# Optimization experiments

Hardware: AMD Instinct MI355X
Metric: run time of the kernel (lower is better)

## Reference

```python
import jax, jax.numpy as jnp
import numpy as np

N, E_EDGES = 100000, 1600000
IN_DIM, HEADS, OUT_DIM = 128, 8, 8


def setup_inputs() -> dict:
    key = jax.random.key(0)
    ks = jax.random.split(key, 12)
    d = HEADS * OUT_DIM
    s = 1.0 / np.sqrt(IN_DIM)
    inp = {
        'x': jax.random.normal(ks[0], (N, IN_DIM), dtype=jnp.float32),
        'edge_attr': jax.random.normal(ks[1], (E_EDGES, 1), dtype=jnp.float32),
        'edge_index': jax.random.randint(ks[2], (2, E_EDGES), 0, N, dtype=jnp.int64),
        'Wq': jax.random.normal(ks[3], (IN_DIM, d), dtype=jnp.float32) * s,
        'bq': jnp.zeros((d,), dtype=jnp.float32),
        'Wk': jax.random.normal(ks[4], (IN_DIM, d), dtype=jnp.float32) * s,
        'bk': jnp.zeros((d,), dtype=jnp.float32),
        'We': jax.random.normal(ks[5], (1, d), dtype=jnp.float32),
        'be': jnp.zeros((d,), dtype=jnp.float32),
        'Wv': jax.random.normal(ks[6], (IN_DIM, d), dtype=jnp.float32) * s,
        'bv': jnp.zeros((d,), dtype=jnp.float32),
    }
    return inp


def reference(x, edge_attr, edge_index, Wq, bq, Wk, bk, We, be, Wv, bv):
    n = x.shape[0]
    # Projections, reshaped to [N, H, D] (and [E, H, D] for edge features)
    Qh = (x @ Wq + bq).reshape(n, HEADS, OUT_DIM)
    Kh = (x @ Wk + bk).reshape(n, HEADS, OUT_DIM)
    Vh = (x @ Wv + bv).reshape(n, HEADS, OUT_DIM)
    Eh = (edge_attr @ We + be).reshape(-1, HEADS, OUT_DIM)

    src = edge_index[0]
    dst = edge_index[1]
    # Per-edge score: (K[src] * Q[dst] / sqrt(D)) * E, summed over D, clamped, exp'd
    score = (Kh[src] * Qh[dst]) * (1.0 / np.sqrt(OUT_DIM)) * Eh  # [E, H, D]
    score = jnp.exp(jnp.clip(jnp.sum(score, axis=-1, keepdims=True), -5.0, 5.0))  # [E, H, 1]

    msg = Vh[src] * score  # [E, H, D]
    wV = jax.ops.segment_sum(msg, dst, num_segments=n)     # [N, H, D]
    Z = jax.ops.segment_sum(score, dst, num_segments=n)    # [N, H, 1]
    return wV / (Z + 1e-6)
```

## Files before the change

kernel.cpp:

```cpp
#include <hip/hip_runtime.h>
#include <math.h>

#define NN 100000
#define EE 1600000
#define IND 128
#define D64 64

#define BSHIFT 8
#define NBUCK 391
#define P1_TILE 3072
#define NB_P1 521

#define QKV_BLOCKS 3125
#define WT_BLOCKS 96

typedef __attribute__((ext_vector_type(8))) short  short8;
typedef __attribute__((ext_vector_type(4))) float  f32x4;

__device__ __forceinline__ unsigned short bf16_rne(float v) {
    unsigned int u = __float_as_uint(v);
    return (unsigned short)((u + 0x7FFFu + ((u >> 16) & 1u)) >> 16);
}

__global__ __launch_bounds__(256) void fusedA_kernel(
    const float* __restrict__ Wq, const float* __restrict__ Wk,
    const float* __restrict__ Wv,
    unsigned short* __restrict__ wt_hi, unsigned short* __restrict__ wt_lo,
    const int* __restrict__ ei, int* __restrict__ hist)
{
    __shared__ int lh[NBUCK];
    const int t = threadIdx.x;

    if (blockIdx.x < WT_BLOCKS) {
        int idx = blockIdx.x * 256 + t;
        int col = idx >> 7, k = idx & 127;
        const float* W = (col < 64) ? Wq : (col < 128) ? Wk : Wv;
        float v = W[(size_t)k * D64 + (col & 63)];
        unsigned short h = bf16_rne(v);
        float hf = __uint_as_float((unsigned int)h << 16);
        unsigned short l = bf16_rne(v - hf);
        wt_hi[idx] = h;
        wt_lo[idx] = l;
        return;
    }

    const int pb = blockIdx.x - WT_BLOCKS;
    for (int b = t; b < NBUCK; b += 256) lh[b] = 0;
    __syncthreads();

    const int e0 = pb * P1_TILE;
#pragma unroll
    for (int j = 0; j < 12; ++j) {
        int e = e0 + j * 256 + t;
        if (e < EE) {
            int d = ei[EE + e];
            atomicAdd(&lh[d >> BSHIFT], 1);
        }
    }
    __syncthreads();
    for (int b = t; b < NBUCK; b += 256)
        hist[pb * NBUCK + b] = lh[b];
}

__global__ __launch_bounds__(256) void hscanA_kernel(int* __restrict__ hist,
                                                     int* __restrict__ btot)
{
    const int b = blockIdx.x;
    const int t = threadIdx.x;
    int L[3]; int s = 0;
#pragma unroll
    for (int j = 0; j < 3; ++j) {
        int blk = t * 3 + j;
        L[j] = (blk < NB_P1) ? hist[blk * NBUCK + b] : 0;
        s += L[j];
    }
    int lane = t & 63, w = t >> 6;
    int incl = s;
    for (int o = 1; o < 64; o <<= 1) {
        int v = __shfl_up(incl, o);
        if (lane >= o) incl += v;
    }
    __shared__ int wsum[4];
    if (lane == 63) wsum[w] = incl;
    __syncthreads();
    int wbase = 0;
#pragma unroll
    for (int i = 0; i < 4; ++i) if (i < w) wbase += wsum[i];
    int run = wbase + incl - s;
#pragma unroll
    for (int j = 0; j < 3; ++j) {
        int blk = t * 3 + j;
        if (blk < NB_P1) hist[blk * NBUCK + b] = run;
        run += L[j];
    }
    if (t == 0) btot[b] = wsum[0] + wsum[1] + wsum[2] + wsum[3];
}

__global__ __launch_bounds__(256) void bscan_kernel(const int* __restrict__ btot,
                                                    int* __restrict__ bbase)
{
    const int t = threadIdx.x;
    int i0 = 2 * t, i1 = 2 * t + 1;
    int v0 = (i0 < NBUCK) ? btot[i0] : 0;
    int v1 = (i1 < NBUCK) ? btot[i1] : 0;
    int s = v0 + v1;
    int lane = t & 63, w = t >> 6;
    int incl = s;
    for (int o = 1; o < 64; o <<= 1) {
        int v = __shfl_up(incl, o);
        if (lane >= o) incl += v;
    }
    __shared__ int wsum[4];
    if (lane == 63) wsum[w] = incl;
    __syncthreads();
    int wbase = 0;
#pragma unroll
    for (int i = 0; i < 4; ++i) if (i < w) wbase += wsum[i];
    int excl = wbase + incl - s;
    if (i0 <= NBUCK) bbase[i0] = excl;
    if (i1 <= NBUCK) bbase[i1] = excl + v0;
}

#define XP 132

__global__ __launch_bounds__(256) void fusedB_kernel(
    const float* __restrict__ x,
    const unsigned short* __restrict__ wt_hi,
    const unsigned short* __restrict__ wt_lo,
    const float* __restrict__ bq, const float* __restrict__ bk,
    const float* __restrict__ bv,
    float* __restrict__ Qo, unsigned int* __restrict__ KVb,
    const int* __restrict__ ei, const float* __restrict__ ea,
    const int* __restrict__ hist, const int* __restrict__ bbase,
    int2* __restrict__ staging)
{
    __shared__ __align__(16) char smem[2 * 32 * XP * 2];

    const int t = threadIdx.x;

    if (blockIdx.x >= QKV_BLOCKS) {
        int* lr = (int*)smem;
        const int pb = blockIdx.x - QKV_BLOCKS;
        for (int b = t; b < NBUCK; b += 256)
            lr[b] = hist[pb * NBUCK + b] + bbase[b];
        __syncthreads();

        const int e0 = pb * P1_TILE;
#pragma unroll
        for (int j = 0; j < 12; ++j) {
            int e = e0 + j * 256 + t;
            if (e < EE) {
                int s = ei[e];
                int d = ei[EE + e];
                int pos = atomicAdd(&lr[d >> BSHIFT], 1);
                staging[pos] = make_int2(s | ((d & 255) << 17), __float_as_int(ea[e]));
            }
        }
        return;
    }

    unsigned short* xhi = (unsigned short*)smem;
    unsigned short* xlo = (unsigned short*)(smem + 32 * XP * 2);

    const int wave = t >> 6;
    const int lane = t & 63;
    const int nb   = blockIdx.x * 32;

    {
        const int row = t >> 3;
        const int c   = t & 7;
        const float* xr = x + (size_t)(nb + row) * IND + c * 16;
        float4 a0 = *(const float4*)(xr);
        float4 a1 = *(const float4*)(xr + 4);
        float4 a2 = *(const float4*)(xr + 8);
        float4 a3 = *(const float4*)(xr + 12);
        float vs[16] = { a0.x, a0.y, a0.z, a0.w, a1.x, a1.y, a1.z, a1.w,
                         a2.x, a2.y, a2.z, a2.w, a3.x, a3.y, a3.z, a3.w };
        short8 h0, h1, l0, l1;
#pragma unroll
        for (int j = 0; j < 8; ++j) {
            unsigned short hb = bf16_rne(vs[j]);
            float hf = __uint_as_float((unsigned int)hb << 16);
            h0[j] = (short)hb;
            l0[j] = (short)bf16_rne(vs[j] - hf);
        }
#pragma unroll
        for (int j = 0; j < 8; ++j) {
            unsigned short hb = bf16_rne(vs[8 + j]);
            float hf = __uint_as_float((unsigned int)hb << 16);
            h1[j] = (short)hb;
            l1[j] = (short)bf16_rne(vs[8 + j] - hf);
        }
        int o0 = row * XP + c * 16;
        *(short8*)&xhi[o0]     = h0;
        *(short8*)&xhi[o0 + 8] = h1;
        *(short8*)&xlo[o0]     = l0;
        *(short8*)&xlo[o0 + 8] = l1;
    }
    __syncthreads();

    const int wcol0 = wave * 48;

    f32x4 acc[2][3];
#pragma unroll
    for (int rt = 0; rt < 2; ++rt)
#pragma unroll
        for (int ct = 0; ct < 3; ++ct)
            acc[rt][ct] = (f32x4){0.f, 0.f, 0.f, 0.f};

#pragma unroll
    for (int kt = 0; kt < 4; ++kt) {
        short8 bh[3], bl[3];
#pragma unroll
        for (int ct = 0; ct < 3; ++ct) {
            int col = wcol0 + ct * 16 + (lane & 15);
            int a = col * 128 + kt * 32 + (lane >> 4) * 8;
            bh[ct] = *(const short8*)&wt_hi[a];
            bl[ct] = *(const short8*)&wt_lo[a];
        }
        short8 ah[2], al[2];
#pragma unroll
        for (int rt = 0; rt < 2; ++rt) {
            int o2 = (rt * 16 + (lane & 15)) * XP + kt * 32 + (lane >> 4) * 8;
            ah[rt] = *(const short8*)&xhi[o2];
            al[rt] = *(const short8*)&xlo[o2];
        }
#pragma unroll
        for (int rt = 0; rt < 2; ++rt) {
#pragma unroll
            for (int ct = 0; ct < 3; ++ct) {
                acc[rt][ct] = __builtin_amdgcn_mfma_f32_16x16x32_bf16(
                    ah[rt], bh[ct], acc[rt][ct], 0, 0, 0);
                acc[rt][ct] = __builtin_amdgcn_mfma_f32_16x16x32_bf16(
                    ah[rt], bl[ct], acc[rt][ct], 0, 0, 0);
                acc[rt][ct] = __builtin_amdgcn_mfma_f32_16x16x32_bf16(
                    al[rt], bh[ct], acc[rt][ct], 0, 0, 0);
            }
        }
    }

#pragma unroll
    for (int ct = 0; ct < 3; ++ct) {
        int colbase = wcol0 + ct * 16;
        int m  = colbase >> 6;
        int lc = (colbase & 63) + (lane & 15);
        const float* bp = (m == 0) ? bq : (m == 1) ? bk : bv;
        float bias = bp[lc];
#pragma unroll
        for (int rt = 0; rt < 2; ++rt) {
#pragma unroll
            for (int reg = 0; reg < 4; ++reg) {
                int node = nb + rt * 16 + (lane >> 4) * 4 + reg;
                float val = acc[rt][ct][reg] + bias;
                size_t idx = (size_t)node * D64 + lc;
                if (m == 0) {
                    Qo[idx] = val;
                } else {
                    ((unsigned short*)KVb)[idx * 2 + (m == 1 ? 1 : 0)] = bf16_rne(val);
                }
            }
        }
    }
}

__global__ __launch_bounds__(256) void p2_kernel(const int2* __restrict__ staging,
                                                 const int* __restrict__ bbase,
                                                 int* __restrict__ off,
                                                 int2* __restrict__ epack)
{
    const int bucket = blockIdx.x;
    const int t      = threadIdx.x;
    const int n0     = bucket << BSHIFT;
    const int sb     = bbase[bucket];
    const int se     = bbase[bucket + 1];

    __shared__ int lcnt[256];
    __shared__ int lcur[256];
    __shared__ int wsum[4];
    lcnt[t] = 0;
    __syncthreads();

    for (int r = sb + t; r < se; r += 256)
        atomicAdd(&lcnt[(staging[r].x >> 17) & 255], 1);
    __syncthreads();

    int cnt  = lcnt[t];
    int lane = t & 63, w = t >> 6;
    int incl = cnt;
    for (int o = 1; o < 64; o <<= 1) {
        int v = __shfl_up(incl, o);
        if (lane >= o) incl += v;
    }
    if (lane == 63) wsum[w] = incl;
    __syncthreads();
    int wbase = 0;
#pragma unroll
    for (int i = 0; i < 4; ++i) if (i < w) wbase += wsum[i];
    int ov = sb + wbase + incl - cnt;

    int node = n0 + t;
    if (node <= NN) off[node] = ov;
    lcur[t] = ov;
    __syncthreads();

    for (int r = sb + t; r < se; r += 256) {
        int2 rec = staging[r];
        int dl = (rec.x >> 17) & 255;
        int pos = atomicAdd(&lcur[dl], 1);
        epack[pos] = make_int2(rec.x & 0x1FFFF, rec.y);
    }
}

__global__ __launch_bounds__(256) void attn_kernel(
    const float* __restrict__ Q, const unsigned int* __restrict__ KVb,
    const int* __restrict__ off, const int2* __restrict__ epack,
    const float* __restrict__ We, const float* __restrict__ be,
    float* __restrict__ out)
{
    const int lane = threadIdx.x & 63;
    const int node = blockIdx.x * 4 + (threadIdx.x >> 6);

    const int h  = lane & 7;
    const int es = lane >> 3;

    float wq[8], bq[8];
    {
        const float4* qp = (const float4*)&Q[(size_t)node * D64 + h * 8];
        float4 q0 = qp[0], q1 = qp[1];
        const float4* wp = (const float4*)&We[h * 8];
        float4 w0 = wp[0], w1 = wp[1];
        const float4* bp = (const float4*)&be[h * 8];
        float4 b0 = bp[0], b1 = bp[1];
        const float rs = 0.35355339059327373f;
        float qs[8] = { q0.x, q0.y, q0.z, q0.w, q1.x, q1.y, q1.z, q1.w };
        float ws[8] = { w0.x, w0.y, w0.z, w0.w, w1.x, w1.y, w1.z, w1.w };
        float bs[8] = { b0.x, b0.y, b0.z, b0.w, b1.x, b1.y, b1.z, b1.w };
#pragma unroll
        for (int d = 0; d < 8; ++d) {
            float qr = qs[d] * rs;
            wq[d] = ws[d] * qr;
            bq[d] = bs[d] * qr;
        }
    }

    const int i0 = off[node];
    const int i1 = off[node + 1];

    float acc[8];
#pragma unroll
    for (int d = 0; d < 8; ++d) acc[d] = 0.f;
    float z = 0.f;

    int i = i0;
#pragma unroll 2
    for (; i + 8 <= i1; i += 8) {
        int2 rec = epack[i + es];
        unsigned int bo = ((unsigned int)rec.x << 6) + (h << 3);
        float attr = __int_as_float(rec.y);

        uint4 wA = *(const uint4*)(KVb + bo);
        uint4 wB = *(const uint4*)(KVb + bo + 4);
        unsigned int wv[8] = { wA.x, wA.y, wA.z, wA.w, wB.x, wB.y, wB.z, wB.w };

        float tt = 0.f;
#pragma unroll
        for (int d = 0; d < 8; ++d) {
            float s  = fmaf(attr, wq[d], bq[d]);
            float kf = __uint_as_float(wv[d] & 0xFFFF0000u);
            tt = fmaf(kf, s, tt);
        }
        tt = fminf(fmaxf(tt, -5.f), 5.f);
        float sc = __expf(tt);

#pragma unroll
        for (int d = 0; d < 8; ++d) {
            float vf = __uint_as_float(wv[d] << 16);
            acc[d] = fmaf(vf, sc, acc[d]);
        }
        z += sc;
    }

    if (i < i1) {
        int  idx   = i + es;
        bool valid = idx < i1;
        int2 rec   = epack[valid ? idx : i0];
        unsigned int bo = ((unsigned int)rec.x << 6) + (h << 3);
        float attr = __int_as_float(rec.y);

        uint4 wA = *(const uint4*)(KVb + bo);
        uint4 wB = *(const uint4*)(KVb + bo + 4);
        unsigned int wv[8] = { wA.x, wA.y, wA.z, wA.w, wB.x, wB.y, wB.z, wB.w };

        float tt = 0.f;
#pragma unroll
        for (int d = 0; d < 8; ++d) {
            float s  = fmaf(attr, wq[d], bq[d]);
            float kf = __uint_as_float(wv[d] & 0xFFFF0000u);
            tt = fmaf(kf, s, tt);
        }
        tt = fminf(fmaxf(tt, -5.f), 5.f);
        float sc = __expf(tt);
        sc = valid ? sc : 0.f;

#pragma unroll
        for (int d = 0; d < 8; ++d) {
            float vf = __uint_as_float(wv[d] << 16);
            acc[d] = fmaf(vf, sc, acc[d]);
        }
        z += sc;
    }

#pragma unroll
    for (int m = 8; m <= 32; m <<= 1) {
#pragma unroll
        for (int d = 0; d < 8; ++d) acc[d] += __shfl_xor(acc[d], m);
        z += __shfl_xor(z, m);
    }

    float val = acc[0];
#pragma unroll
    for (int j = 1; j < 8; ++j)
        val = (es == j) ? acc[j] : val;

    out[(size_t)node * D64 + h * 8 + es] = val / (z + 1e-6f);
}

static inline size_t align256(size_t v) { return (v + 255) & ~(size_t)255; }

extern "C" void kernel_launch(void* const* d_in, const int* in_sizes, int n_in,
                              void* d_out, int out_size, void* d_ws, size_t ws_size,
                              hipStream_t stream)
{
    const float* x  = (const float*)d_in[0];
    const float* ea = (const float*)d_in[1];
    const int*   ei = (const int*)  d_in[2];
    const float* Wq = (const float*)d_in[3];
    const float* bq = (const float*)d_in[4];
    const float* Wk = (const float*)d_in[5];
    const float* bk = (const float*)d_in[6];
    const float* We = (const float*)d_in[7];
    const float* be = (const float*)d_in[8];
    const float* Wv = (const float*)d_in[9];
    const float* bv = (const float*)d_in[10];
    float* out = (float*)d_out;

    char* ws = (char*)d_ws;
    size_t o = 0;
    float*          Q       = (float*)(ws + o);          o += align256((size_t)NN * D64 * 4);
    unsigned int*   KVb     = (unsigned int*)(ws + o);   o += align256((size_t)NN * D64 * 4);
    int*            off     = (int*)(ws + o);            o += align256((size_t)(NN + 1) * 4);
    unsigned short* wt_hi   = (unsigned short*)(ws + o); o += align256((size_t)192 * 128 * 2);
    unsigned short* wt_lo   = (unsigned short*)(ws + o); o += align256((size_t)192 * 128 * 2);
    int*            hist    = (int*)(ws + o);            o += align256((size_t)NB_P1 * NBUCK * 4);
    int*            btot    = (int*)(ws + o);            o += align256((size_t)NBUCK * 4);
    int*            bbase   = (int*)(ws + o);            o += align256((size_t)(NBUCK + 1) * 4);
    int2*           staging = (int2*)(ws + o);           o += align256((size_t)EE * 8);
    int2*           epack   = (int2*)(ws + o);           o += align256((size_t)EE * 8);
    (void)ws_size; (void)out_size; (void)in_sizes; (void)n_in;

    fusedA_kernel<<<WT_BLOCKS + NB_P1, 256, 0, stream>>>(Wq, Wk, Wv, wt_hi, wt_lo, ei, hist);
    hscanA_kernel<<<NBUCK, 256, 0, stream>>>(hist, btot);
    bscan_kernel<<<1, 256, 0, stream>>>(btot, bbase);
    fusedB_kernel<<<QKV_BLOCKS + NB_P1, 256, 0, stream>>>(x, wt_hi, wt_lo, bq, bk, bv,
                                                          Q, KVb, ei, ea, hist, bbase, staging);
    p2_kernel<<<NBUCK, 256, 0, stream>>>(staging, bbase, off, epack);
    attn_kernel<<<NN / 4, 256, 0, stream>>>(Q, KVb, off, epack, We, be, out);
}
```

Baseline: 156.1 us.

## Persist QKV blocks over four tiles with register prefetch of next x tile

The QKV projection blocks now each process four 32-row tiles in a loop, and the next tile's x rows are loaded into registers while the current tile runs its MFMAs, so global load latency overlaps with compute. The scatter (p1) blocks are moved to the front of the grid so they get scheduled first, and the LDS row pitch changes from 132 to 136 to alter the bank mapping. The cost is fewer blocks, which lowers parallelism for load balancing, plus an extra barrier per tile and more live registers.

```diff
diff --git a/kernel.cpp b/kernel.cpp
--- a/kernel.cpp
+++ b/kernel.cpp
@@ -11,7 +11,9 @@
 #define P1_TILE 3072
 #define NB_P1 521
 
-#define QKV_BLOCKS 3125
+#define QKV_TILES 3125
+#define QKV_TPB 4
+#define QKV_BLOCKS_F 782
 #define WT_BLOCKS 96
 
 typedef __attribute__((ext_vector_type(8))) short  short8;
@@ -121,7 +123,7 @@
     if (i1 <= NBUCK) bbase[i1] = excl + v0;
 }
 
-#define XP 132
+#define XP 136
 
 __global__ __launch_bounds__(256) void fusedB_kernel(
     const float* __restrict__ x,
@@ -138,9 +140,9 @@
 
     const int t = threadIdx.x;
 
-    if (blockIdx.x >= QKV_BLOCKS) {
+    if (blockIdx.x < NB_P1) {
         int* lr = (int*)smem;
-        const int pb = blockIdx.x - QKV_BLOCKS;
+        const int pb = blockIdx.x;
         for (int b = t; b < NBUCK; b += 256)
             lr[b] = hist[pb * NBUCK + b] + bbase[b];
         __syncthreads();
@@ -162,101 +164,126 @@
     unsigned short* xhi = (unsigned short*)smem;
     unsigned short* xlo = (unsigned short*)(smem + 32 * XP * 2);
 
+    const int qb   = blockIdx.x - NB_P1;
     const int wave = t >> 6;
     const int lane = t & 63;
-    const int nb   = blockIdx.x * 32;
-
+    const int row  = t >> 3;
+    const int c    = t & 7;
+    const int wcol0 = wave * 48;
+
+    float4 ra, rb, rc, rd;
     {
-        const int row = t >> 3;
-        const int c   = t & 7;
-        const float* xr = x + (size_t)(nb + row) * IND + c * 16;
-        float4 a0 = *(const float4*)(xr);
-        float4 a1 = *(const float4*)(xr + 4);
-        float4 a2 = *(const float4*)(xr + 8);
-        float4 a3 = *(const float4*)(xr + 12);
-        float vs[16] = { a0.x, a0.y, a0.z, a0.w, a1.x, a1.y, a1.z, a1.w,
-                         a2.x, a2.y, a2.z, a2.w, a3.x, a3.y, a3.z, a3.w };
-        short8 h0, h1, l0, l1;
-#pragma unroll
-        for (int j = 0; j < 8; ++j) {
-            unsigned short hb = bf16_rne(vs[j]);
-            float hf = __uint_as_float((unsigned int)hb << 16);
-            h0[j] = (short)hb;
-            l0[j] = (short)bf16_rne(vs[j] - hf);
-        }
-#pragma unroll
-        for (int j = 0; j < 8; ++j) {
-            unsigned short hb = bf16_rne(vs[8 + j]);
-            float hf = __uint_as_float((unsigned int)hb << 16);
-            h1[j] = (short)hb;
-            l1[j] = (short)bf16_rne(vs[8 + j] - hf);
-        }
-        int o0 = row * XP + c * 16;
-        *(short8*)&xhi[o0]     = h0;
-        *(short8*)&xhi[o0 + 8] = h1;
-        *(short8*)&xlo[o0]     = l0;
-        *(short8*)&xlo[o0 + 8] = l1;
-    }
-    __syncthreads();
-
-    const int wcol0 = wave * 48;
-
-    f32x4 acc[2][3];
-#pragma unroll
-    for (int rt = 0; rt < 2; ++rt)
-#pragma unroll
-        for (int ct = 0; ct < 3; ++ct)
-            acc[rt][ct] = (f32x4){0.f, 0.f, 0.f, 0.f};
-
-#pragma unroll
-    for (int kt = 0; kt < 4; ++kt) {
-        short8 bh[3], bl[3];
+        int tl = qb * QKV_TPB;
+        if (tl < QKV_TILES) {
+            const float* xr = x + (size_t)(tl * 32 + row) * IND + c * 16;
+            ra = *(const float4*)(xr);
+            rb = *(const float4*)(xr + 4);
+            rc = *(const float4*)(xr + 8);
+            rd = *(const float4*)(xr + 12);
+        }
+    }
+
+    for (int it = 0; it < QKV_TPB; ++it) {
+        const int tl = qb * QKV_TPB + it;
+        if (tl >= QKV_TILES) break;
+        const int nb = tl * 32;
+
+        if (it > 0) __syncthreads();
+
+        {
+            float vs[16] = { ra.x, ra.y, ra.z, ra.w, rb.x, rb.y, rb.z, rb.w,
+                             rc.x, rc.y, rc.z, rc.w, rd.x, rd.y, rd.z, rd.w };
+            short8 h0, h1, l0, l1;
+#pragma unroll
+            for (int j = 0; j < 8; ++j) {
+                unsigned short hb = bf16_rne(vs[j]);
+                float hf = __uint_as_float((unsigned int)hb << 16);
+                h0[j] = (short)hb;
+                l0[j] = (short)bf16_rne(vs[j] - hf);
+            }
+#pragma unroll
+            for (int j = 0; j < 8; ++j) {
+                unsigned short hb = bf16_rne(vs[8 + j]);
+                float hf = __uint_as_float((unsigned int)hb << 16);
+                h1[j] = (short)hb;
+                l1[j] = (short)bf16_rne(vs[8 + j] - hf);
+            }
+            int o0 = row * XP + c * 16;
+            *(short8*)&xhi[o0]     = h0;
+            *(short8*)&xhi[o0 + 8] = h1;
+            *(short8*)&xlo[o0]     = l0;
+            *(short8*)&xlo[o0 + 8] = l1;
+        }
+        __syncthreads();
+
+        {
+            int tn = tl + 1;
+            if (it + 1 < QKV_TPB && tn < QKV_TILES) {
+                const float* xr = x + (size_t)(tn * 32 + row) * IND + c * 16;
+                ra = *(const float4*)(xr);
+                rb = *(const float4*)(xr + 4);
+                rc = *(const float4*)(xr + 8);
+                rd = *(const float4*)(xr + 12);
+            }
+        }
+
+        f32x4 acc[2][3];
+#pragma unroll
+        for (int rt = 0; rt < 2; ++rt)
+#pragma unroll
+            for (int ct = 0; ct < 3; ++ct)
+                acc[rt][ct] = (f32x4){0.f, 0.f, 0.f, 0.f};
+
+#pragma unroll
+        for (int kt = 0; kt < 4; ++kt) {
+            short8 bh[3], bl[3];
+#pragma unroll
+            for (int ct = 0; ct < 3; ++ct) {
+                int col = wcol0 + ct * 16 + (lane & 15);
+                int a = col * 128 + kt * 32 + (lane >> 4) * 8;
+                bh[ct] = *(const short8*)&wt_hi[a];
+                bl[ct] = *(const short8*)&wt_lo[a];
+            }
+            short8 ah[2], al[2];
+#pragma unroll
+            for (int rt = 0; rt < 2; ++rt) {
+                int o2 = (rt * 16 + (lane & 15)) * XP + kt * 32 + (lane >> 4) * 8;
+                ah[rt] = *(const short8*)&xhi[o2];
+                al[rt] = *(const short8*)&xlo[o2];
+            }
+#pragma unroll
+            for (int rt = 0; rt < 2; ++rt) {
+#pragma unroll
+                for (int ct = 0; ct < 3; ++ct) {
+                    acc[rt][ct] = __builtin_amdgcn_mfma_f32_16x16x32_bf16(
+                        ah[rt], bh[ct], acc[rt][ct], 0, 0, 0);
+                    acc[rt][ct] = __builtin_amdgcn_mfma_f32_16x16x32_bf16(
+                        ah[rt], bl[ct], acc[rt][ct], 0, 0, 0);
+                    acc[rt][ct] = __builtin_amdgcn_mfma_f32_16x16x32_bf16(
+                        al[rt], bh[ct], acc[rt][ct], 0, 0, 0);
+                }
+            }
+        }
+
 #pragma unroll
         for (int ct = 0; ct < 3; ++ct) {
-            int col = wcol0 + ct * 16 + (lane & 15);
-            int a = col * 128 + kt * 32 + (lane >> 4) * 8;
-            bh[ct] = *(const short8*)&wt_hi[a];
-            bl[ct] = *(const short8*)&wt_lo[a];
-        }
-        short8 ah[2], al[2];
-#pragma unroll
-        for (int rt = 0; rt < 2; ++rt) {
-            int o2 = (rt * 16 + (lane & 15)) * XP + kt * 32 + (lane >> 4) * 8;
-            ah[rt] = *(const short8*)&xhi[o2];
-            al[rt] = *(const short8*)&xlo[o2];
-        }
-#pragma unroll
-        for (int rt = 0; rt < 2; ++rt) {
-#pragma unroll
-            for (int ct = 0; ct < 3; ++ct) {
-                acc[rt][ct] = __builtin_amdgcn_mfma_f32_16x16x32_bf16(
-                    ah[rt], bh[ct], acc[rt][ct], 0, 0, 0);
-                acc[rt][ct] = __builtin_amdgcn_mfma_f32_16x16x32_bf16(
-                    ah[rt], bl[ct], acc[rt][ct], 0, 0, 0);
-                acc[rt][ct] = __builtin_amdgcn_mfma_f32_16x16x32_bf16(
-                    al[rt], bh[ct], acc[rt][ct], 0, 0, 0);
-            }
-        }
-    }
-
-#pragma unroll
-    for (int ct = 0; ct < 3; ++ct) {
-        int colbase = wcol0 + ct * 16;
-        int m  = colbase >> 6;
-        int lc = (colbase & 63) + (lane & 15);
-        const float* bp = (m == 0) ? bq : (m == 1) ? bk : bv;
-        float bias = bp[lc];
-#pragma unroll
-        for (int rt = 0; rt < 2; ++rt) {
-#pragma unroll
-            for (int reg = 0; reg < 4; ++reg) {
-                int node = nb + rt * 16 + (lane >> 4) * 4 + reg;
-                float val = acc[rt][ct][reg] + bias;
-                size_t idx = (size_t)node * D64 + lc;
-                if (m == 0) {
-                    Qo[idx] = val;
-                } else {
-                    ((unsigned short*)KVb)[idx * 2 + (m == 1 ? 1 : 0)] = bf16_rne(val);
+            int colbase = wcol0 + ct * 16;
+            int m  = colbase >> 6;
+            int lc = (colbase & 63) + (lane & 15);
+            const float* bp = (m == 0) ? bq : (m == 1) ? bk : bv;
+            float bias = bp[lc];
+#pragma unroll
+            for (int rt = 0; rt < 2; ++rt) {
+#pragma unroll
+                for (int reg = 0; reg < 4; ++reg) {
+                    int node = nb + rt * 16 + (lane >> 4) * 4 + reg;
+                    float val = acc[rt][ct][reg] + bias;
+                    size_t idx = (size_t)node * D64 + lc;
+                    if (m == 0) {
+                        Qo[idx] = val;
+                    } else {
+                        ((unsigned short*)KVb)[idx * 2 + (m == 1 ? 1 : 0)] = bf16_rne(val);
+                    }
                 }
             }
         }
@@ -461,8 +488,8 @@
     fusedA_kernel<<<WT_BLOCKS + NB_P1, 256, 0, stream>>>(Wq, Wk, Wv, wt_hi, wt_lo, ei, hist);
     hscanA_kernel<<<NBUCK, 256, 0, stream>>>(hist, btot);
     bscan_kernel<<<1, 256, 0, stream>>>(btot, bbase);
-    fusedB_kernel<<<QKV_BLOCKS + NB_P1, 256, 0, stream>>>(x, wt_hi, wt_lo, bq, bk, bv,
-                                                          Q, KVb, ei, ea, hist, bbase, staging);
+    fusedB_kernel<<<NB_P1 + QKV_BLOCKS_F, 256, 0, stream>>>(x, wt_hi, wt_lo, bq, bk, bv,
+                                                            Q, KVb, ei, ea, hist, bbase, staging);
     p2_kernel<<<NBUCK, 256, 0, stream>>>(staging, bbase, off, epack);
     attn_kernel<<<NN / 4, 256, 0, stream>>>(Q, KVb, off, epack, We, be, out);
 }
```

Measured after the change: 169.4 us. +8.5%, slower.

## Restructure QKV projection to per-wave 16-row tiles without LDS staging

Applied to the files above, without the earlier changes.

The fused projection kernel now drops to 128-thread blocks. Each wave loads its own 16 rows of x directly into registers, splits them into bf16 hi/lo, and computes all 192 output columns, so the shared-memory staging and the barrier go away. K and V are packed into one 32-bit store per element, and the scatter blocks are reordered to come first in the grid so they launch early. In exchange, each wave reads the full weight matrix from global/L2 and holds 12 accumulators, which raises register pressure.

```diff
diff --git a/kernel.cpp b/kernel.cpp
--- a/kernel.cpp
+++ b/kernel.cpp
@@ -121,9 +121,7 @@
     if (i1 <= NBUCK) bbase[i1] = excl + v0;
 }
 
-#define XP 132
-
-__global__ __launch_bounds__(256) void fusedB_kernel(
+__global__ __launch_bounds__(128) void fusedB_kernel(
     const float* __restrict__ x,
     const unsigned short* __restrict__ wt_hi,
     const unsigned short* __restrict__ wt_lo,
@@ -134,21 +132,19 @@
     const int* __restrict__ hist, const int* __restrict__ bbase,
     int2* __restrict__ staging)
 {
-    __shared__ __align__(16) char smem[2 * 32 * XP * 2];
-
+    __shared__ int lr[NBUCK];
     const int t = threadIdx.x;
 
-    if (blockIdx.x >= QKV_BLOCKS) {
-        int* lr = (int*)smem;
-        const int pb = blockIdx.x - QKV_BLOCKS;
-        for (int b = t; b < NBUCK; b += 256)
+    if (blockIdx.x < NB_P1) {
+        const int pb = blockIdx.x;
+        for (int b = t; b < NBUCK; b += 128)
             lr[b] = hist[pb * NBUCK + b] + bbase[b];
         __syncthreads();
 
         const int e0 = pb * P1_TILE;
 #pragma unroll
-        for (int j = 0; j < 12; ++j) {
-            int e = e0 + j * 256 + t;
+        for (int j = 0; j < 24; ++j) {
+            int e = e0 + j * 128 + t;
             if (e < EE) {
                 int s = ei[e];
                 int d = ei[EE + e];
@@ -159,106 +155,71 @@
         return;
     }
 
-    unsigned short* xhi = (unsigned short*)smem;
-    unsigned short* xlo = (unsigned short*)(smem + 32 * XP * 2);
-
+    const int qb   = blockIdx.x - NB_P1;
     const int wave = t >> 6;
     const int lane = t & 63;
-    const int nb   = blockIdx.x * 32;
-
-    {
-        const int row = t >> 3;
-        const int c   = t & 7;
-        const float* xr = x + (size_t)(nb + row) * IND + c * 16;
-        float4 a0 = *(const float4*)(xr);
-        float4 a1 = *(const float4*)(xr + 4);
-        float4 a2 = *(const float4*)(xr + 8);
-        float4 a3 = *(const float4*)(xr + 12);
-        float vs[16] = { a0.x, a0.y, a0.z, a0.w, a1.x, a1.y, a1.z, a1.w,
-                         a2.x, a2.y, a2.z, a2.w, a3.x, a3.y, a3.z, a3.w };
-        short8 h0, h1, l0, l1;
+    const int nb16 = qb * 32 + wave * 16;
+    const int nr   = lane & 15;
+    const int q4   = lane >> 4;
+
+    const float* xr = x + (size_t)(nb16 + nr) * IND + q4 * 8;
+    float4 xa[4][2];
+#pragma unroll
+    for (int kt = 0; kt < 4; ++kt) {
+        xa[kt][0] = *(const float4*)(xr + kt * 32);
+        xa[kt][1] = *(const float4*)(xr + kt * 32 + 4);
+    }
+
+    float biasq[4], biask[4], biasv[4];
+#pragma unroll
+    for (int j = 0; j < 4; ++j) {
+        biasq[j] = bq[j * 16 + nr];
+        biask[j] = bk[j * 16 + nr];
+        biasv[j] = bv[j * 16 + nr];
+    }
+
+    f32x4 acc[12];
+#pragma unroll
+    for (int c = 0; c < 12; ++c) acc[c] = (f32x4){0.f, 0.f, 0.f, 0.f};
+
+#pragma unroll
+    for (int kt = 0; kt < 4; ++kt) {
+        float vs[8] = { xa[kt][0].x, xa[kt][0].y, xa[kt][0].z, xa[kt][0].w,
+                        xa[kt][1].x, xa[kt][1].y, xa[kt][1].z, xa[kt][1].w };
+        short8 ah, al;
 #pragma unroll
         for (int j = 0; j < 8; ++j) {
             unsigned short hb = bf16_rne(vs[j]);
             float hf = __uint_as_float((unsigned int)hb << 16);
-            h0[j] = (short)hb;
-            l0[j] = (short)bf16_rne(vs[j] - hf);
-        }
-#pragma unroll
-        for (int j = 0; j < 8; ++j) {
-            unsigned short hb = bf16_rne(vs[8 + j]);
-            float hf = __uint_as_float((unsigned int)hb << 16);
-            h1[j] = (short)hb;
-            l1[j] = (short)bf16_rne(vs[8 + j] - hf);
-        }
-        int o0 = row * XP + c * 16;
-        *(short8*)&xhi[o0]     = h0;
-        *(short8*)&xhi[o0 + 8] = h1;
-        *(short8*)&xlo[o0]     = l0;
-        *(short8*)&xlo[o0 + 8] = l1;
-    }
-    __syncthreads();
-
-    const int wcol0 = wave * 48;
-
-    f32x4 acc[2][3];
-#pragma unroll
-    for (int rt = 0; rt < 2; ++rt)
-#pragma unroll
-        for (int ct = 0; ct < 3; ++ct)
-            acc[rt][ct] = (f32x4){0.f, 0.f, 0.f, 0.f};
-
-#pragma unroll
-    for (int kt = 0; kt < 4; ++kt) {
-        short8 bh[3], bl[3];
-#pragma unroll
-        for (int ct = 0; ct < 3; ++ct) {
-            int col = wcol0 + ct * 16 + (lane & 15);
-            int a = col * 128 + kt * 32 + (lane >> 4) * 8;
-            bh[ct] = *(const short8*)&wt_hi[a];
-            bl[ct] = *(const short8*)&wt_lo[a];
-        }
-        short8 ah[2], al[2];
-#pragma unroll
-        for (int rt = 0; rt < 2; ++rt) {
-            int o2 = (rt * 16 + (lane & 15)) * XP + kt * 32 + (lane >> 4) * 8;
-            ah[rt] = *(const short8*)&xhi[o2];
-            al[rt] = *(const short8*)&xlo[o2];
-        }
-#pragma unroll
-        for (int rt = 0; rt < 2; ++rt) {
-#pragma unroll
-            for (int ct = 0; ct < 3; ++ct) {
-                acc[rt][ct] = __builtin_amdgcn_mfma_f32_16x16x32_bf16(
-                    ah[rt], bh[ct], acc[rt][ct], 0, 0, 0);
-                acc[rt][ct] = __builtin_amdgcn_mfma_f32_16x16x32_bf16(
-                    ah[rt], bl[ct], acc[rt][ct], 0, 0, 0);
-                acc[rt][ct] = __builtin_amdgcn_mfma_f32_16x16x32_bf16(
-                    al[rt], bh[ct], acc[rt][ct], 0, 0, 0);
-            }
-        }
-    }
-
-#pragma unroll
-    for (int ct = 0; ct < 3; ++ct) {
-        int colbase = wcol0 + ct * 16;
-        int m  = colbase >> 6;
-        int lc = (colbase & 63) + (lane & 15);
-        const float* bp = (m == 0) ? bq : (m == 1) ? bk : bv;
-        float bias = bp[lc];
-#pragma unroll
-        for (int rt = 0; rt < 2; ++rt) {
-#pragma unroll
-            for (int reg = 0; reg < 4; ++reg) {
-                int node = nb + rt * 16 + (lane >> 4) * 4 + reg;
-                float val = acc[rt][ct][reg] + bias;
-                size_t idx = (size_t)node * D64 + lc;
-                if (m == 0) {
-                    Qo[idx] = val;
-                } else {
-                    ((unsigned short*)KVb)[idx * 2 + (m == 1 ? 1 : 0)] = bf16_rne(val);
-                }
-            }
+            ah[j] = (short)hb;
+            al[j] = (short)bf16_rne(vs[j] - hf);
+        }
+#pragma unroll
+        for (int ct = 0; ct < 12; ++ct) {
+            int col = ct * 16 + nr;
+            int a = col * 128 + kt * 32 + q4 * 8;
+            short8 bh = *(const short8*)&wt_hi[a];
+            short8 bl = *(const short8*)&wt_lo[a];
+            acc[ct] = __builtin_amdgcn_mfma_f32_16x16x32_bf16(ah, bh, acc[ct], 0, 0, 0);
+            acc[ct] = __builtin_amdgcn_mfma_f32_16x16x32_bf16(ah, bl, acc[ct], 0, 0, 0);
+            acc[ct] = __builtin_amdgcn_mfma_f32_16x16x32_bf16(al, bh, acc[ct], 0, 0, 0);
+        }
+    }
+
+#pragma unroll
+    for (int j = 0; j < 4; ++j) {
+#pragma unroll
+        for (int reg = 0; reg < 4; ++reg) {
+            int node = nb16 + q4 * 4 + reg;
+            Qo[(size_t)node * D64 + j * 16 + nr] = acc[j][reg] + biasq[j];
+        }
+#pragma unroll
+        for (int reg = 0; reg < 4; ++reg) {
+            int node = nb16 + q4 * 4 + reg;
+            float kv = acc[4 + j][reg] + biask[j];
+            float vv = acc[8 + j][reg] + biasv[j];
+            unsigned int pk = ((unsigned int)bf16_rne(kv) << 16) | bf16_rne(vv);
+            KVb[(size_t)node * D64 + j * 16 + nr] = pk;
         }
     }
 }
@@ -461,7 +422,7 @@
     fusedA_kernel<<<WT_BLOCKS + NB_P1, 256, 0, stream>>>(Wq, Wk, Wv, wt_hi, wt_lo, ei, hist);
     hscanA_kernel<<<NBUCK, 256, 0, stream>>>(hist, btot);
     bscan_kernel<<<1, 256, 0, stream>>>(btot, bbase);
-    fusedB_kernel<<<QKV_BLOCKS + NB_P1, 256, 0, stream>>>(x, wt_hi, wt_lo, bq, bk, bv,
+    fusedB_kernel<<<NB_P1 + QKV_BLOCKS, 128, 0, stream>>>(x, wt_hi, wt_lo, bq, bk, bv,
                                                           Q, KVb, ei, ea, hist, bbase, staging);
     p2_kernel<<<NBUCK, 256, 0, stream>>>(staging, bbase, off, epack);
     attn_kernel<<<NN / 4, 256, 0, stream>>>(Q, KVb, off, epack, We, be, out);
```

Result: slower. 186.6 us (+19.5%).
